# Performance work log

Hardware: AMD Instinct MI355X
Metric: run time of the kernel (lower is better)

The kernel has to match this reference:

```python
import jax, jax.numpy as jnp
import numpy as np

B, S, D, H = 2, 2048, 1024, 16  # batch, seq, embed_dim, num_heads
DH = D // H                      # head dim = 64


def setup_inputs() -> dict:
    key = jax.random.key(0)
    kx, kq, kbq, kk, kbk, kv, kbv = jax.random.split(key, 7)
    scale = 1.0 / np.sqrt(D)
    return {
        "x": jax.random.normal(kx, (B, S, D), dtype=jnp.float32),
        "Wq": jax.random.normal(kq, (D, D), dtype=jnp.float32) * scale,
        "bq": jax.random.normal(kbq, (D,), dtype=jnp.float32) * 0.01,
        "Wk": jax.random.normal(kk, (D, D), dtype=jnp.float32) * scale,
        "bk": jax.random.normal(kbk, (D,), dtype=jnp.float32) * 0.01,
        "Wv": jax.random.normal(kv, (D, D), dtype=jnp.float32) * scale,
        "bv": jax.random.normal(kbv, (D,), dtype=jnp.float32) * 0.01,
    }


def reference(x, Wq, bq, Wk, bk, Wv, bv):
    # ooqkv_type == 'q', odeint_method == 'id': q branch = act(Linear(x)), exact GELU (torch nn.GELU default)
    q = jax.nn.gelu(x @ Wq + bq, approximate=False)
    k = x @ Wk + bk
    v = x @ Wv + bv
    # [B, S, D] -> [B, S, H, DH]
    q = q.reshape(B, S, H, DH)
    k = k.reshape(B, S, H, DH)
    v = v.reshape(B, S, H, DH)
    # NOTE: original module has NO 1/sqrt(d) scale — faithful reproduction
    att = jnp.einsum("bqhd,bkhd->bhqk", q, k)
    att = jax.nn.softmax(att, axis=-1)
    out = jnp.einsum("bhqk,bkhd->bqhd", att, v)
    return out.reshape(B, S, D)
```

## Files before the change

### kernel.cpp

```cpp
#include <hip/hip_runtime.h>
#include <math.h>

#define B_  2
#define S_  2048
#define D_  1024
#define H_  16
#define DH_ 64
#define M_  (B_ * S_)

typedef _Float16 half_t;
typedef __attribute__((ext_vector_type(8))) _Float16 h8;
typedef __attribute__((ext_vector_type(4))) _Float16 h4;
typedef __attribute__((ext_vector_type(4))) float   f32x4;

#define LOG2E 1.44269504088896f

__device__ __forceinline__ void gll16(const half_t* g, half_t* l) {
    __builtin_amdgcn_global_load_lds(
        (__attribute__((address_space(1))) const void*)g,
        (__attribute__((address_space(3))) void*)l, 16, 0, 0);
}

__global__ __launch_bounds__(256) void prep_k(
    const float* __restrict__ x, half_t* __restrict__ xh,
    const float* __restrict__ Wq, const float* __restrict__ Wk,
    const float* __restrict__ Wv, half_t* __restrict__ Wt)
{
    const int bx = blockIdx.x;
    if (bx < 2048) {
        const size_t i = ((size_t)bx * 256 + threadIdx.x) * 8;
        const float4 a = *(const float4*)(x + i);
        const float4 b = *(const float4*)(x + i + 4);
        h8 o;
        o[0] = (half_t)a.x; o[1] = (half_t)a.y; o[2] = (half_t)a.z; o[3] = (half_t)a.w;
        o[4] = (half_t)b.x; o[5] = (half_t)b.y; o[6] = (half_t)b.z; o[7] = (half_t)b.w;
        *(h8*)(xh + i) = o;
    } else {
        const int gb    = bx - 2048;
        const int which = gb >> 9;
        const float* __restrict__ W = (which == 0) ? Wq : (which == 1) ? Wk : Wv;
        half_t* __restrict__ T = Wt + (size_t)which * D_ * D_;
        const int gw   = (gb & 511) * 4 + (threadIdx.x >> 6);
        const int lane = threadIdx.x & 63;
        const int n    = (gw & 15) * 64 + lane;
        const int k0   = (gw >> 4) * 8;
        h8 o;
        #pragma unroll
        for (int t = 0; t < 8; ++t) o[t] = (half_t)W[(size_t)(k0 + t) * D_ + n];
        *(h8*)(T + (size_t)n * D_ + k0) = o;
    }
}

__global__ __launch_bounds__(256) void qkv_gemm_f16(
    const half_t* __restrict__ xh, const half_t* __restrict__ Wt,
    const float* __restrict__ bq, const float* __restrict__ bk,
    const float* __restrict__ bv,
    half_t* __restrict__ Qo, half_t* __restrict__ Ko, half_t* __restrict__ Vt)
{
    const int n0g   = blockIdx.x * 128;
    const int which = n0g >> 10;
    const int n0    = n0g & 1023;
    const int m0    = blockIdx.y * 128;
    const half_t* __restrict__ Wp  = Wt + (size_t)which * D_ * D_;
    const float* __restrict__ bias = (which == 0) ? bq : (which == 1) ? bk : bv;

    const int tid = threadIdx.x, lane = tid & 63, wave = tid >> 6;
    const int wm = (wave >> 1) * 64, wn = (wave & 1) * 64;
    const int ln = lane & 15, quad = lane >> 4;

    __shared__ __align__(16) half_t As[128 * 64];
    __shared__ __align__(16) half_t Bs[128 * 64];

    f32x4 acc[4][4];
    #pragma unroll
    for (int i = 0; i < 4; ++i)
        #pragma unroll
        for (int j = 0; j < 4; ++j) acc[i][j] = (f32x4){0.f, 0.f, 0.f, 0.f};

    for (int k0 = 0; k0 < D_; k0 += 64) {
        __syncthreads();
        #pragma unroll
        for (int l = 0; l < 4; ++l) {
            const int c  = tid + l * 256;
            const int r  = c >> 3, c0 = c & 7;
            const int cs = c0 ^ (r & 7);
            gll16(xh + (size_t)(m0 + r) * D_ + k0 + cs * 8, &As[c * 8]);
            gll16(Wp + (size_t)(n0 + r) * D_ + k0 + cs * 8, &Bs[c * 8]);
        }
        __syncthreads();

        #pragma unroll
        for (int kc = 0; kc < 2; ++kc) {
            h8 af[4], bf[4];
            #pragma unroll
            for (int i = 0; i < 4; ++i) {
                const int r = wm + i * 16 + ln;
                af[i] = *(const h8*)&As[r * 64 + (((kc << 2) + quad) ^ (r & 7)) * 8];
            }
            #pragma unroll
            for (int j = 0; j < 4; ++j) {
                const int r = wn + j * 16 + ln;
                bf[j] = *(const h8*)&Bs[r * 64 + (((kc << 2) + quad) ^ (r & 7)) * 8];
            }
            #pragma unroll
            for (int i = 0; i < 4; ++i)
                #pragma unroll
                for (int j = 0; j < 4; ++j)
                    acc[i][j] = __builtin_amdgcn_mfma_f32_16x16x32_f16(
                        af[i], bf[j], acc[i][j], 0, 0, 0);
        }
    }

    if (which == 2) {
        #pragma unroll
        for (int j = 0; j < 4; ++j) {
            const int col = n0 + wn + j * 16 + ln;
            const int h = col >> 6, d = col & 63;
            const float bb = bias[col];
            #pragma unroll
            for (int i = 0; i < 4; ++i) {
                const int sg = m0 + wm + i * 16 + quad * 4;
                const int b  = sg >> 11, srow = sg & 2047;
                h4 pv;
                #pragma unroll
                for (int r = 0; r < 4; ++r) pv[r] = (half_t)(acc[i][j][r] + bb);
                *(h4*)(Vt + (((size_t)(b * H_ + h) * DH_ + d) * S_ + srow)) = pv;
            }
        }
    } else {
        half_t* __restrict__ out = (which == 0) ? Qo : Ko;
        #pragma unroll
        for (int j = 0; j < 4; ++j) {
            const int col = n0 + wn + j * 16 + ln;
            const float bb = bias[col];
            #pragma unroll
            for (int i = 0; i < 4; ++i) {
                #pragma unroll
                for (int r = 0; r < 4; ++r) {
                    const int row = m0 + wm + i * 16 + quad * 4 + r;
                    float t = acc[i][j][r] + bb;
                    if (which == 0) {
                        const float u = t * fmaf(t * t, 0.0356774081f, 0.7978845608f);
                        const float e = __builtin_amdgcn_exp2f(u * -2.88539008178f);
                        t = t * __builtin_amdgcn_rcpf(1.0f + e) * LOG2E;
                    }
                    out[(size_t)row * D_ + col] = (half_t)t;
                }
            }
        }
    }
}

__global__ __launch_bounds__(256) void attn_f16(
    const half_t* __restrict__ Q, const half_t* __restrict__ K,
    const half_t* __restrict__ Vt, float* __restrict__ out)
{
    const int tid  = threadIdx.x;
    const int lane = tid & 63;
    const int wave = tid >> 6;
    const int ln   = lane & 15;
    const int quad = lane >> 4;
    const int bh   = blockIdx.y;
    const int b    = bh >> 4;
    const int h    = bh & 15;
    const int q0   = blockIdx.x * 128;

    const half_t* __restrict__ Qb  = Q  + (size_t)b * S_ * D_ + h * DH_;
    const half_t* __restrict__ Kb  = K  + (size_t)b * S_ * D_ + h * DH_;
    const half_t* __restrict__ Vtb = Vt + (size_t)bh * DH_ * S_;

    __shared__ __align__(16) half_t Ks[64 * 64];
    __shared__ __align__(16) half_t Vs[64 * 64];
    __shared__ __align__(16) half_t QPs[128][72];

    #pragma unroll
    for (int l = 0; l < 4; ++l) {
        const int c = tid + l * 256;
        const int r = c >> 3, k8 = c & 7;
        *(h8*)&QPs[r][k8 * 8] = *(const h8*)(Qb + (size_t)(q0 + r) * D_ + k8 * 8);
    }
    __syncthreads();
    const h8 qa0 = *(const h8*)&QPs[wave * 32 + ln][quad * 8];
    const h8 qa1 = *(const h8*)&QPs[wave * 32 + ln][32 + quad * 8];
    const h8 qc0 = *(const h8*)&QPs[wave * 32 + 16 + ln][quad * 8];
    const h8 qc1 = *(const h8*)&QPs[wave * 32 + 16 + ln][32 + quad * 8];

    h8 ones8;
    #pragma unroll
    for (int t = 0; t < 8; ++t) ones8[t] = (half_t)1.0f;

    f32x4 Oa[4], Ob[4];
    #pragma unroll
    for (int j = 0; j < 4; ++j) {
        Oa[j] = (f32x4){0.f, 0.f, 0.f, 0.f};
        Ob[j] = (f32x4){0.f, 0.f, 0.f, 0.f};
    }
    f32x4 la = (f32x4){0.f, 0.f, 0.f, 0.f};
    f32x4 lb = (f32x4){0.f, 0.f, 0.f, 0.f};
    float m_a = -INFINITY, m_b = -INFINITY;

    for (int k0 = 0; k0 < S_; k0 += 64) {
        __syncthreads();
        #pragma unroll
        for (int l = 0; l < 2; ++l) {
            const int c  = tid + l * 256;
            const int r  = c >> 3, c0 = c & 7;
            const int cs = c0 ^ (r & 7);
            gll16(Kb  + (size_t)(k0 + r) * D_ + cs * 8, &Ks[c * 8]);
            gll16(Vtb + (size_t)r * S_ + k0 + cs * 8,   &Vs[c * 8]);
        }
        __syncthreads();

        f32x4 sa[4], sb[4];
        #pragma unroll
        for (int j = 0; j < 4; ++j) {
            const int rK = j * 16 + ln;
            const h8 ka0 = *(const h8*)&Ks[rK * 64 + ((quad)     ^ (rK & 7)) * 8];
            const h8 ka1 = *(const h8*)&Ks[rK * 64 + ((quad + 4) ^ (rK & 7)) * 8];
            f32x4 t = (f32x4){0.f, 0.f, 0.f, 0.f};
            t = __builtin_amdgcn_mfma_f32_16x16x32_f16(ka0, qa0, t, 0, 0, 0);
            t = __builtin_amdgcn_mfma_f32_16x16x32_f16(ka1, qa1, t, 0, 0, 0);
            sa[j] = t;
            f32x4 u = (f32x4){0.f, 0.f, 0.f, 0.f};
            u = __builtin_amdgcn_mfma_f32_16x16x32_f16(ka0, qc0, u, 0, 0, 0);
            u = __builtin_amdgcn_mfma_f32_16x16x32_f16(ka1, qc1, u, 0, 0, 0);
            sb[j] = u;
        }

        float mxa = sa[0][0], mxb = sb[0][0];
        #pragma unroll
        for (int j = 0; j < 4; ++j)
            #pragma unroll
            for (int r = 0; r < 4; ++r) {
                mxa = fmaxf(mxa, sa[j][r]);
                mxb = fmaxf(mxb, sb[j][r]);
            }
        mxa = fmaxf(mxa, __shfl_xor(mxa, 16, 64));
        mxa = fmaxf(mxa, __shfl_xor(mxa, 32, 64));
        mxb = fmaxf(mxb, __shfl_xor(mxb, 16, 64));
        mxb = fmaxf(mxb, __shfl_xor(mxb, 32, 64));

        if (__ballot(mxa > m_a || mxb > m_b)) {
            const float mna = fmaxf(m_a, mxa);
            const float mnb = fmaxf(m_b, mxb);
            const float ala = __builtin_amdgcn_exp2f(m_a - mna);
            const float alb = __builtin_amdgcn_exp2f(m_b - mnb);
            m_a = mna; m_b = mnb;
            float ra[4], rb[4];
            #pragma unroll
            for (int r = 0; r < 4; ++r) {
                ra[r] = __shfl(ala, quad * 4 + r, 64);
                rb[r] = __shfl(alb, quad * 4 + r, 64);
            }
            #pragma unroll
            for (int r = 0; r < 4; ++r) {
                la[r] *= ra[r]; lb[r] *= rb[r];
                #pragma unroll
                for (int j = 0; j < 4; ++j) { Oa[j][r] *= ra[r]; Ob[j][r] *= rb[r]; }
            }
        }

        #pragma unroll
        for (int j = 0; j < 4; ++j) {
            h4 pva, pvb;
            #pragma unroll
            for (int r = 0; r < 4; ++r) {
                pva[r] = (half_t)__builtin_amdgcn_exp2f(sa[j][r] - m_a);
                pvb[r] = (half_t)__builtin_amdgcn_exp2f(sb[j][r] - m_b);
            }
            *(h4*)&QPs[wave * 32 + ln][j * 16 + quad * 4]      = pva;
            *(h4*)&QPs[wave * 32 + 16 + ln][j * 16 + quad * 4] = pvb;
        }

        const h8 pa0 = *(const h8*)&QPs[wave * 32 + ln][quad * 8];
        const h8 pa1 = *(const h8*)&QPs[wave * 32 + ln][32 + quad * 8];
        const h8 pb0 = *(const h8*)&QPs[wave * 32 + 16 + ln][quad * 8];
        const h8 pb1 = *(const h8*)&QPs[wave * 32 + 16 + ln][32 + quad * 8];
        #pragma unroll
        for (int j = 0; j < 4; ++j) {
            const int rV = j * 16 + ln;
            const h8 vb0 = *(const h8*)&Vs[rV * 64 + ((quad)     ^ (rV & 7)) * 8];
            const h8 vb1 = *(const h8*)&Vs[rV * 64 + ((quad + 4) ^ (rV & 7)) * 8];
            Oa[j] = __builtin_amdgcn_mfma_f32_16x16x32_f16(pa0, vb0, Oa[j], 0, 0, 0);
            Oa[j] = __builtin_amdgcn_mfma_f32_16x16x32_f16(pa1, vb1, Oa[j], 0, 0, 0);
            Ob[j] = __builtin_amdgcn_mfma_f32_16x16x32_f16(pb0, vb0, Ob[j], 0, 0, 0);
            Ob[j] = __builtin_amdgcn_mfma_f32_16x16x32_f16(pb1, vb1, Ob[j], 0, 0, 0);
        }
        la = __builtin_amdgcn_mfma_f32_16x16x32_f16(pa0, ones8, la, 0, 0, 0);
        la = __builtin_amdgcn_mfma_f32_16x16x32_f16(pa1, ones8, la, 0, 0, 0);
        lb = __builtin_amdgcn_mfma_f32_16x16x32_f16(pb0, ones8, lb, 0, 0, 0);
        lb = __builtin_amdgcn_mfma_f32_16x16x32_f16(pb1, ones8, lb, 0, 0, 0);
    }

    #pragma unroll
    for (int r = 0; r < 4; ++r) {
        const float iva = 1.0f / la[r];
        const float ivb = 1.0f / lb[r];
        const int rowa = q0 + wave * 32 + quad * 4 + r;
        const int rowb = rowa + 16;
        #pragma unroll
        for (int j = 0; j < 4; ++j) {
            out[((size_t)b * S_ + rowa) * D_ + h * DH_ + j * 16 + ln] = Oa[j][r] * iva;
            out[((size_t)b * S_ + rowb) * D_ + h * DH_ + j * 16 + ln] = Ob[j][r] * ivb;
        }
    }
}

extern "C" void kernel_launch(void* const* d_in, const int* in_sizes, int n_in,
                              void* d_out, int out_size, void* d_ws, size_t ws_size,
                              hipStream_t stream) {
    const float* x  = (const float*)d_in[0];
    const float* Wq = (const float*)d_in[1];
    const float* bq = (const float*)d_in[2];
    const float* Wk = (const float*)d_in[3];
    const float* bk = (const float*)d_in[4];
    const float* Wv = (const float*)d_in[5];
    const float* bv = (const float*)d_in[6];
    float* out = (float*)d_out;

    const size_t nmd = (size_t)M_ * D_;
    const size_t ndd = (size_t)D_ * D_;
    half_t* xh  = (half_t*)d_ws;
    half_t* Wt  = xh + nmd;
    half_t* Qh  = Wt + 3 * ndd;
    half_t* Kh  = Qh + nmd;
    half_t* Vtw = Kh + nmd;

    prep_k<<<2048 + 1536, 256, 0, stream>>>(x, xh, Wq, Wk, Wv, Wt);
    qkv_gemm_f16<<<dim3(3 * D_ / 128, M_ / 128), 256, 0, stream>>>(
        xh, Wt, bq, bk, bv, Qh, Kh, Vtw);
    attn_f16<<<dim3(S_ / 128, B_ * H_), 256, 0, stream>>>(Qh, Kh, Vtw, out);
}
```

Measured before the change: 196.0 us.

## Load K/V directly from global memory and remap blocks for XCD-aware locality

The attention kernel no longer stages K and V tiles in shared memory. Each wave loads its K and V fragments straight from global memory into registers, which removes both block barriers per iteration. Both kernels switch to a 1D grid with a swizzled block index, so blocks that share a head or an M-tile land on the same XCD and can reuse its L2. The trade-off is redundant global/L2 traffic (every wave reloads the same K/V), uncoalesced 16-byte row loads, and higher register pressure.

```diff
diff --git a/kernel.cpp b/kernel.cpp
--- a/kernel.cpp
+++ b/kernel.cpp
@@ -57,10 +57,13 @@
     const float* __restrict__ bv,
     half_t* __restrict__ Qo, half_t* __restrict__ Ko, half_t* __restrict__ Vt)
 {
-    const int n0g   = blockIdx.x * 128;
+    const int bi = blockIdx.x;
+    const int mt = (bi & 7) * 4 + ((bi >> 3) & 3);
+    const int nt = bi >> 5;
+    const int m0 = mt * 128;
+    const int n0g = nt * 128;
     const int which = n0g >> 10;
     const int n0    = n0g & 1023;
-    const int m0    = blockIdx.y * 128;
     const half_t* __restrict__ Wp  = Wt + (size_t)which * D_ * D_;
     const float* __restrict__ bias = (which == 0) ? bq : (which == 1) ? bk : bv;
 
@@ -160,30 +163,24 @@
     const int wave = tid >> 6;
     const int ln   = lane & 15;
     const int quad = lane >> 4;
-    const int bh   = blockIdx.y;
-    const int b    = bh >> 4;
-    const int h    = bh & 15;
-    const int q0   = blockIdx.x * 128;
+
+    const int bi = blockIdx.x;
+    const int bh = (bi & 7) * 4 + ((bi >> 3) & 3);
+    const int q0 = (bi >> 5) * 128;
+    const int b  = bh >> 4;
+    const int h  = bh & 15;
 
     const half_t* __restrict__ Qb  = Q  + (size_t)b * S_ * D_ + h * DH_;
     const half_t* __restrict__ Kb  = K  + (size_t)b * S_ * D_ + h * DH_;
     const half_t* __restrict__ Vtb = Vt + (size_t)bh * DH_ * S_;
 
-    __shared__ __align__(16) half_t Ks[64 * 64];
-    __shared__ __align__(16) half_t Vs[64 * 64];
-    __shared__ __align__(16) half_t QPs[128][72];
-
-    #pragma unroll
-    for (int l = 0; l < 4; ++l) {
-        const int c = tid + l * 256;
-        const int r = c >> 3, k8 = c & 7;
-        *(h8*)&QPs[r][k8 * 8] = *(const h8*)(Qb + (size_t)(q0 + r) * D_ + k8 * 8);
-    }
-    __syncthreads();
-    const h8 qa0 = *(const h8*)&QPs[wave * 32 + ln][quad * 8];
-    const h8 qa1 = *(const h8*)&QPs[wave * 32 + ln][32 + quad * 8];
-    const h8 qc0 = *(const h8*)&QPs[wave * 32 + 16 + ln][quad * 8];
-    const h8 qc1 = *(const h8*)&QPs[wave * 32 + 16 + ln][32 + quad * 8];
+    __shared__ __align__(16) half_t Ps[128][72];
+
+    const int qra = q0 + wave * 32 + ln;
+    const h8 qa0 = *(const h8*)(Qb + (size_t)qra * D_ + quad * 8);
+    const h8 qa1 = *(const h8*)(Qb + (size_t)qra * D_ + 32 + quad * 8);
+    const h8 qc0 = *(const h8*)(Qb + (size_t)(qra + 16) * D_ + quad * 8);
+    const h8 qc1 = *(const h8*)(Qb + (size_t)(qra + 16) * D_ + 32 + quad * 8);
 
     h8 ones8;
     #pragma unroll
@@ -200,31 +197,33 @@
     float m_a = -INFINITY, m_b = -INFINITY;
 
     for (int k0 = 0; k0 < S_; k0 += 64) {
-        __syncthreads();
-        #pragma unroll
-        for (int l = 0; l < 2; ++l) {
-            const int c  = tid + l * 256;
-            const int r  = c >> 3, c0 = c & 7;
-            const int cs = c0 ^ (r & 7);
-            gll16(Kb  + (size_t)(k0 + r) * D_ + cs * 8, &Ks[c * 8]);
-            gll16(Vtb + (size_t)r * S_ + k0 + cs * 8,   &Vs[c * 8]);
-        }
-        __syncthreads();
+        h8 ka0[4], ka1[4];
+        #pragma unroll
+        for (int j = 0; j < 4; ++j) {
+            const half_t* kp = Kb + (size_t)(k0 + j * 16 + ln) * D_;
+            ka0[j] = *(const h8*)(kp + quad * 8);
+            ka1[j] = *(const h8*)(kp + 32 + quad * 8);
+        }
 
         f32x4 sa[4], sb[4];
         #pragma unroll
         for (int j = 0; j < 4; ++j) {
-            const int rK = j * 16 + ln;
-            const h8 ka0 = *(const h8*)&Ks[rK * 64 + ((quad)     ^ (rK & 7)) * 8];
-            const h8 ka1 = *(const h8*)&Ks[rK * 64 + ((quad + 4) ^ (rK & 7)) * 8];
             f32x4 t = (f32x4){0.f, 0.f, 0.f, 0.f};
-            t = __builtin_amdgcn_mfma_f32_16x16x32_f16(ka0, qa0, t, 0, 0, 0);
-            t = __builtin_amdgcn_mfma_f32_16x16x32_f16(ka1, qa1, t, 0, 0, 0);
+            t = __builtin_amdgcn_mfma_f32_16x16x32_f16(ka0[j], qa0, t, 0, 0, 0);
+            t = __builtin_amdgcn_mfma_f32_16x16x32_f16(ka1[j], qa1, t, 0, 0, 0);
             sa[j] = t;
             f32x4 u = (f32x4){0.f, 0.f, 0.f, 0.f};
-            u = __builtin_amdgcn_mfma_f32_16x16x32_f16(ka0, qc0, u, 0, 0, 0);
-            u = __builtin_amdgcn_mfma_f32_16x16x32_f16(ka1, qc1, u, 0, 0, 0);
+            u = __builtin_amdgcn_mfma_f32_16x16x32_f16(ka0[j], qc0, u, 0, 0, 0);
+            u = __builtin_amdgcn_mfma_f32_16x16x32_f16(ka1[j], qc1, u, 0, 0, 0);
             sb[j] = u;
+        }
+
+        h8 vb0[4], vb1[4];
+        #pragma unroll
+        for (int j = 0; j < 4; ++j) {
+            const half_t* vp = Vtb + (size_t)(j * 16 + ln) * S_ + k0;
+            vb0[j] = *(const h8*)(vp + quad * 8);
+            vb1[j] = *(const h8*)(vp + 32 + quad * 8);
         }
 
         float mxa = sa[0][0], mxb = sb[0][0];
@@ -268,23 +267,20 @@
                 pva[r] = (half_t)__builtin_amdgcn_exp2f(sa[j][r] - m_a);
                 pvb[r] = (half_t)__builtin_amdgcn_exp2f(sb[j][r] - m_b);
             }
-            *(h4*)&QPs[wave * 32 + ln][j * 16 + quad * 4]      = pva;
-            *(h4*)&QPs[wave * 32 + 16 + ln][j * 16 + quad * 4] = pvb;
-        }
-
-        const h8 pa0 = *(const h8*)&QPs[wave * 32 + ln][quad * 8];
-        const h8 pa1 = *(const h8*)&QPs[wave * 32 + ln][32 + quad * 8];
-        const h8 pb0 = *(const h8*)&QPs[wave * 32 + 16 + ln][quad * 8];
-        const h8 pb1 = *(const h8*)&QPs[wave * 32 + 16 + ln][32 + quad * 8];
-        #pragma unroll
-        for (int j = 0; j < 4; ++j) {
-            const int rV = j * 16 + ln;
-            const h8 vb0 = *(const h8*)&Vs[rV * 64 + ((quad)     ^ (rV & 7)) * 8];
-            const h8 vb1 = *(const h8*)&Vs[rV * 64 + ((quad + 4) ^ (rV & 7)) * 8];
-            Oa[j] = __builtin_amdgcn_mfma_f32_16x16x32_f16(pa0, vb0, Oa[j], 0, 0, 0);
-            Oa[j] = __builtin_amdgcn_mfma_f32_16x16x32_f16(pa1, vb1, Oa[j], 0, 0, 0);
-            Ob[j] = __builtin_amdgcn_mfma_f32_16x16x32_f16(pb0, vb0, Ob[j], 0, 0, 0);
-            Ob[j] = __builtin_amdgcn_mfma_f32_16x16x32_f16(pb1, vb1, Ob[j], 0, 0, 0);
+            *(h4*)&Ps[wave * 32 + ln][j * 16 + quad * 4]      = pva;
+            *(h4*)&Ps[wave * 32 + 16 + ln][j * 16 + quad * 4] = pvb;
+        }
+
+        const h8 pa0 = *(const h8*)&Ps[wave * 32 + ln][quad * 8];
+        const h8 pa1 = *(const h8*)&Ps[wave * 32 + ln][32 + quad * 8];
+        const h8 pb0 = *(const h8*)&Ps[wave * 32 + 16 + ln][quad * 8];
+        const h8 pb1 = *(const h8*)&Ps[wave * 32 + 16 + ln][32 + quad * 8];
+        #pragma unroll
+        for (int j = 0; j < 4; ++j) {
+            Oa[j] = __builtin_amdgcn_mfma_f32_16x16x32_f16(pa0, vb0[j], Oa[j], 0, 0, 0);
+            Oa[j] = __builtin_amdgcn_mfma_f32_16x16x32_f16(pa1, vb1[j], Oa[j], 0, 0, 0);
+            Ob[j] = __builtin_amdgcn_mfma_f32_16x16x32_f16(pb0, vb0[j], Ob[j], 0, 0, 0);
+            Ob[j] = __builtin_amdgcn_mfma_f32_16x16x32_f16(pb1, vb1[j], Ob[j], 0, 0, 0);
         }
         la = __builtin_amdgcn_mfma_f32_16x16x32_f16(pa0, ones8, la, 0, 0, 0);
         la = __builtin_amdgcn_mfma_f32_16x16x32_f16(pa1, ones8, la, 0, 0, 0);
@@ -327,7 +323,6 @@
     half_t* Vtw = Kh + nmd;
 
     prep_k<<<2048 + 1536, 256, 0, stream>>>(x, xh, Wq, Wk, Wv, Wt);
-    qkv_gemm_f16<<<dim3(3 * D_ / 128, M_ / 128), 256, 0, stream>>>(
-        xh, Wt, bq, bk, bv, Qh, Kh, Vtw);
-    attn_f16<<<dim3(S_ / 128, B_ * H_), 256, 0, stream>>>(Qh, Kh, Vtw, out);
-}
+    qkv_gemm_f16<<<768, 256, 0, stream>>>(xh, Wt, bq, bk, bv, Qh, Kh, Vtw);
+    attn_f16<<<512, 256, 0, stream>>>(Qh, Kh, Vtw, out);
+}
```

Result: slower. 245.7 us (+25.4%).
